# Performance work log

Hardware: AMD Instinct MI355X
Metric: run time of the kernel (lower is better)

## Reference

```python
import jax, jax.numpy as jnp
import numpy as np

EMBED_DIM = 512
NUM_HEADS = 8
HEAD_DIM = EMBED_DIM // NUM_HEADS
SHIFT_INIT = 5.0
EPS = 1e-6


def setup_inputs() -> dict:
    key = jax.random.key(0)
    ks = jax.random.split(key, 8)
    L, N, E = 2048, 4, EMBED_DIM
    query = jax.random.normal(ks[0], (L, N, E), dtype=jnp.float32)
    k_in = jax.random.normal(ks[1], (L, N, E), dtype=jnp.float32)
    v_in = jax.random.normal(ks[2], (L, N, E), dtype=jnp.float32)
    # MultiheadAttention packed projections
    in_proj_weight = jax.random.normal(ks[3], (3 * E, E), dtype=jnp.float32) / np.sqrt(E)
    in_proj_bias = jnp.zeros((3 * E,), dtype=jnp.float32)
    out_proj_weight = jax.random.normal(ks[4], (E, E), dtype=jnp.float32) / np.sqrt(E)
    out_proj_bias = jnp.zeros((E,), dtype=jnp.float32)
    # GeM parameters: p ~ N(1, 0.02), shift = 5
    p = 1.0 + 0.02 * jax.random.normal(ks[5], (E,), dtype=jnp.float32)
    shift = jnp.full((E,), SHIFT_INIT, dtype=jnp.float32)
    return {
        "query": query, "key": k_in, "value": v_in,
        "in_proj_weight": in_proj_weight, "in_proj_bias": in_proj_bias,
        "out_proj_weight": out_proj_weight, "out_proj_bias": out_proj_bias,
        "p": p, "shift": shift,
    }


def reference(query, key, value, in_proj_weight, in_proj_bias,
              out_proj_weight, out_proj_bias, p, shift):
    L, N, E = query.shape
    H, D = NUM_HEADS, HEAD_DIM
    w_q, w_k, w_v = jnp.split(in_proj_weight, 3, axis=0)   # each (E, E)
    b_q, b_k, b_v = jnp.split(in_proj_bias, 3, axis=0)

    def proj(x, w, b):
        # (L, N, E) -> (N, H, L, D)
        y = x @ w.T + b
        return y.reshape(L, N, H, D).transpose(1, 2, 0, 3)

    q = proj(query, w_q, b_q)
    k = proj(key, w_k, b_k)
    v = proj(value, w_v, b_v)

    scale = 1.0 / np.sqrt(D)
    scores = jnp.einsum('nhld,nhsd->nhls', q, k) * scale   # (N,H,L,S)
    attn = jax.nn.softmax(scores, axis=-1)

    # GeM pooling of values: shift -> power p -> weighted mean -> inverse power -> unshift
    p_h = p.reshape(H, D)[None, :, None, :]                # (1,H,1,D)
    shift_h = shift.reshape(H, D)[None, :, None, :]
    v_pos = jnp.maximum(v + shift_h, EPS)                  # keep base positive
    pooled = jnp.einsum('nhls,nhsd->nhld', attn, v_pos ** p_h)
    out_h = jnp.maximum(pooled, EPS) ** (1.0 / p_h) - shift_h  # (N,H,L,D)

    out = out_h.transpose(2, 0, 1, 3).reshape(L, N, E)     # back to (L,N,E)
    out = out @ out_proj_weight.T + out_proj_bias
    return out
```

## Files before the change

### kernel.cpp

```cpp
#include <hip/hip_runtime.h>
#include <hip/hip_bf16.h>

#define E_DIM 512
#define N_BATCH 4
#define L_SEQ 2048
#define N_HEADS 8
#define H_DIM 64
#define N_ROWS (L_SEQ * N_BATCH)
#define EPS_F 1e-6f

typedef __attribute__((ext_vector_type(8))) short bf16x8;
typedef __attribute__((ext_vector_type(4))) float f32x4;
typedef __attribute__((ext_vector_type(16))) float f32x16;

__device__ __forceinline__ void split2(float f, __hip_bfloat16& h, __hip_bfloat16& l) {
  h = __float2bfloat16(f);
  l = __float2bfloat16(f - __bfloat162float(h));
}

__global__ __launch_bounds__(256) void wconv_kernel(
    const float* __restrict__ wio, const float* __restrict__ wo,
    __hip_bfloat16* __restrict__ wiohi, __hip_bfloat16* __restrict__ wiolo,
    __hip_bfloat16* __restrict__ wohi, __hip_bfloat16* __restrict__ wolo) {
  const int g = blockIdx.x * 256 + threadIdx.x;
  const float* src;
  __hip_bfloat16 *dh, *dl;
  int i;
  if (g < 196608) { src = wio; dh = wiohi; dl = wiolo; i = g * 4; }
  else            { src = wo;  dh = wohi;  dl = wolo;  i = (g - 196608) * 4; }
  const float4 f = *(const float4*)(src + i);
  alignas(8) __hip_bfloat16 h[4], l[4];
  split2(f.x, h[0], l[0]); split2(f.y, h[1], l[1]);
  split2(f.z, h[2], l[2]); split2(f.w, h[3], l[3]);
  *(uint2*)(dh + i) = *(const uint2*)h;
  *(uint2*)(dl + i) = *(const uint2*)l;
}

__global__ __launch_bounds__(256, 3) void proj_qkv_kernel(
    const float* __restrict__ xq, const float* __restrict__ xk,
    const float* __restrict__ xv,
    const __hip_bfloat16* __restrict__ whi, const __hip_bfloat16* __restrict__ wlo,
    const float* __restrict__ bias, const float* __restrict__ pw,
    const float* __restrict__ sw,
    __hip_bfloat16* __restrict__ qbuf, __hip_bfloat16* __restrict__ kbuf,
    float* __restrict__ ubuf) {
  __shared__ __hip_bfloat16 Xh[128][40];
  __shared__ __hip_bfloat16 Xl[128][40];
  __shared__ __hip_bfloat16 Wh[128][40];
  __shared__ __hip_bfloat16 Wl[128][40];
  const int z = blockIdx.z;
  const int row0 = blockIdx.x * 128;
  const int col0 = blockIdx.y * 128;
  const float* __restrict__ xsrc = (z == 0) ? xq : (z == 1) ? xk : xv;
  const int tid = threadIdx.x;
  const int lane = tid & 63;
  const int wv = tid >> 6;
  const int lidx = lane & 15;
  const int quad = lane >> 4;
  const int srow = tid >> 1;
  const int scol = (tid & 1) * 16;

  f32x4 acc[2][8];
#pragma unroll
  for (int rt = 0; rt < 2; ++rt)
#pragma unroll
    for (int ct = 0; ct < 8; ++ct) acc[rt][ct] = (f32x4){0.f, 0.f, 0.f, 0.f};

  const int ar0 = wv * 32 + lidx;

  for (int kt = 0; kt < 16; ++kt) {
    const int k0 = kt * 32;
    {
      const float* xp = xsrc + (size_t)(row0 + srow) * E_DIM + k0 + scol;
      float f[16];
      *(float4*)&f[0]  = ((const float4*)xp)[0];
      *(float4*)&f[4]  = ((const float4*)xp)[1];
      *(float4*)&f[8]  = ((const float4*)xp)[2];
      *(float4*)&f[12] = ((const float4*)xp)[3];
      alignas(16) __hip_bfloat16 hi[16], lo[16];
#pragma unroll
      for (int j = 0; j < 16; ++j) split2(f[j], hi[j], lo[j]);
      *(uint4*)&Xh[srow][scol]     = ((const uint4*)hi)[0];
      *(uint4*)&Xh[srow][scol + 8] = ((const uint4*)hi)[1];
      *(uint4*)&Xl[srow][scol]     = ((const uint4*)lo)[0];
      *(uint4*)&Xl[srow][scol + 8] = ((const uint4*)lo)[1];
    }
    {
      const size_t wof = (size_t)(z * E_DIM + col0 + srow) * E_DIM + k0 + scol;
      *(uint4*)&Wh[srow][scol]     = ((const uint4*)(whi + wof))[0];
      *(uint4*)&Wh[srow][scol + 8] = ((const uint4*)(whi + wof))[1];
      *(uint4*)&Wl[srow][scol]     = ((const uint4*)(wlo + wof))[0];
      *(uint4*)&Wl[srow][scol + 8] = ((const uint4*)(wlo + wof))[1];
    }
    __syncthreads();

    const bf16x8 ah0 = *(const bf16x8*)&Xh[ar0][quad * 8];
    const bf16x8 ah1 = *(const bf16x8*)&Xh[ar0 + 16][quad * 8];
    const bf16x8 al0 = *(const bf16x8*)&Xl[ar0][quad * 8];
    const bf16x8 al1 = *(const bf16x8*)&Xl[ar0 + 16][quad * 8];
#pragma unroll
    for (int ct = 0; ct < 8; ++ct) {
      const bf16x8 bh = *(const bf16x8*)&Wh[ct * 16 + lidx][quad * 8];
      const bf16x8 bl = *(const bf16x8*)&Wl[ct * 16 + lidx][quad * 8];
      acc[0][ct] = __builtin_amdgcn_mfma_f32_16x16x32_bf16(ah0, bh, acc[0][ct], 0, 0, 0);
      acc[0][ct] = __builtin_amdgcn_mfma_f32_16x16x32_bf16(al0, bh, acc[0][ct], 0, 0, 0);
      acc[0][ct] = __builtin_amdgcn_mfma_f32_16x16x32_bf16(ah0, bl, acc[0][ct], 0, 0, 0);
      acc[1][ct] = __builtin_amdgcn_mfma_f32_16x16x32_bf16(ah1, bh, acc[1][ct], 0, 0, 0);
      acc[1][ct] = __builtin_amdgcn_mfma_f32_16x16x32_bf16(al1, bh, acc[1][ct], 0, 0, 0);
      acc[1][ct] = __builtin_amdgcn_mfma_f32_16x16x32_bf16(ah1, bl, acc[1][ct], 0, 0, 0);
    }
    __syncthreads();
  }

  if (z < 2) {
    __hip_bfloat16* __restrict__ dst = (z == 0) ? qbuf : kbuf;
    float bv[8];
#pragma unroll
    for (int ct = 0; ct < 8; ++ct) bv[ct] = bias[z * E_DIM + col0 + ct * 16 + lidx];
#pragma unroll
    for (int rt = 0; rt < 2; ++rt)
#pragma unroll
      for (int ct = 0; ct < 8; ++ct) {
        const int e = col0 + ct * 16 + lidx;
        const int h = e >> 6, d = e & 63;
#pragma unroll
        for (int reg = 0; reg < 4; ++reg) {
          const int R = row0 + wv * 32 + rt * 16 + quad * 4 + reg;
          const int lpos = R >> 2, nb = R & 3;
          dst[(((size_t)nb * N_HEADS + h) * L_SEQ + lpos) * H_DIM + d] =
              __float2bfloat16(acc[rt][ct][reg] + bv[ct]);
        }
      }
  } else {
    float bv[8], pv[8], sv[8];
#pragma unroll
    for (int ct = 0; ct < 8; ++ct) {
      const int e = col0 + ct * 16 + lidx;
      bv[ct] = bias[2 * E_DIM + e]; pv[ct] = pw[e]; sv[ct] = sw[e];
    }
#pragma unroll
    for (int rt = 0; rt < 2; ++rt)
#pragma unroll
      for (int ct = 0; ct < 8; ++ct) {
        const int e = col0 + ct * 16 + lidx;
        const int h = e >> 6, d = e & 63;
#pragma unroll
        for (int reg = 0; reg < 4; ++reg) {
          const int R = row0 + wv * 32 + rt * 16 + quad * 4 + reg;
          const int lpos = R >> 2, nb = R & 3;
          const float y = acc[rt][ct][reg] + bv[ct];
          const float vp = fmaxf(y + sv[ct], EPS_F);
          ubuf[(((size_t)nb * N_HEADS + h) * L_SEQ + lpos) * H_DIM + d] =
              __powf(vp, pv[ct]);
        }
      }
  }
}

__global__ __launch_bounds__(256) void transp_kernel(
    const float* __restrict__ u, __hip_bfloat16* __restrict__ uThi,
    __hip_bfloat16* __restrict__ uTlo) {
  __shared__ float T[64][65];
  const int lt = blockIdx.x, h = blockIdx.y, nb = blockIdx.z;
  const int tid = threadIdx.x;
  const int r = tid >> 2;
  const int cb = (tid & 3) * 16;
  const size_t srcbase = ((size_t)nb * N_HEADS + h) * L_SEQ + lt * 64;
  {
    const float* p = u + (srcbase + r) * H_DIM + cb;
    *(float4*)&T[r][cb + 0]  = ((const float4*)p)[0];
    *(float4*)&T[r][cb + 4]  = ((const float4*)p)[1];
    *(float4*)&T[r][cb + 8]  = ((const float4*)p)[2];
    *(float4*)&T[r][cb + 12] = ((const float4*)p)[3];
  }
  __syncthreads();
  alignas(16) __hip_bfloat16 hi[16], lo[16];
#pragma unroll
  for (int j = 0; j < 16; ++j) split2(T[cb + j][r], hi[j], lo[j]);
  const size_t dst = (((size_t)nb * N_HEADS + h) * H_DIM + r) * L_SEQ + lt * 64 + cb;
  *(uint4*)(uThi + dst)     = ((const uint4*)hi)[0];
  *(uint4*)(uThi + dst + 8) = ((const uint4*)hi)[1];
  *(uint4*)(uTlo + dst)     = ((const uint4*)lo)[0];
  *(uint4*)(uTlo + dst + 8) = ((const uint4*)lo)[1];
}

__global__ __launch_bounds__(128, 2) void attn_kernel(
    const __hip_bfloat16* __restrict__ qbuf, const __hip_bfloat16* __restrict__ kbuf,
    const __hip_bfloat16* __restrict__ uThi, const __hip_bfloat16* __restrict__ uTlo,
    const float* __restrict__ pw, const float* __restrict__ sw,
    __hip_bfloat16* __restrict__ ohhi, __hip_bfloat16* __restrict__ ohlo) {
  __shared__ __hip_bfloat16 Ps[64][72];
  __shared__ __hip_bfloat16 Ks[64][72];
  __shared__ __hip_bfloat16 Uh[64][72];
  __shared__ __hip_bfloat16 Ul[64][72];

  const int qt = blockIdx.x, h = blockIdx.y, nb = blockIdx.z;
  const int q0 = qt * 64;
  const int tid = threadIdx.x;
  const int lane = tid & 63;
  const int wv = tid >> 6;
  const int lm = lane & 31;
  const int kg = lane >> 5;
  const int srow = tid >> 1;
  const int scb = (tid & 1) * 32;

  const size_t headbase = ((size_t)nb * N_HEADS + h) * L_SEQ;
  const size_t dbase = ((size_t)nb * N_HEADS + h) * H_DIM;

  {
    const __hip_bfloat16* p = qbuf + (headbase + q0 + srow) * H_DIM + scb;
    *(uint4*)&Ps[srow][scb + 0]  = ((const uint4*)p)[0];
    *(uint4*)&Ps[srow][scb + 8]  = ((const uint4*)p)[1];
    *(uint4*)&Ps[srow][scb + 16] = ((const uint4*)p)[2];
    *(uint4*)&Ps[srow][scb + 24] = ((const uint4*)p)[3];
  }
  __syncthreads();
  bf16x8 aq[4];
#pragma unroll
  for (int kc = 0; kc < 4; ++kc)
    aq[kc] = *(const bf16x8*)&Ps[wv * 32 + lm][kc * 16 + kg * 8];

  bf16x8 ones;
#pragma unroll
  for (int j = 0; j < 8; ++j) ones[j] = (short)0x3F80;

  float pwv[2], swv[2];
#pragma unroll
  for (int nt = 0; nt < 2; ++nt) {
    const int e = h * H_DIM + nt * 32 + lm;
    pwv[nt] = 1.0f / pw[e];
    swv[nt] = sw[e];
  }

  f32x16 o[2], lacc;
  o[0] = (f32x16)(0.f); o[1] = (f32x16)(0.f); lacc = (f32x16)(0.f);

  for (int scn = 0; scn < 32; ++scn) {
    const int s0 = scn * 64;
    __syncthreads();
    {
      const __hip_bfloat16* kp = kbuf + (headbase + s0 + srow) * H_DIM + scb;
      *(uint4*)&Ks[srow][scb + 0]  = ((const uint4*)kp)[0];
      *(uint4*)&Ks[srow][scb + 8]  = ((const uint4*)kp)[1];
      *(uint4*)&Ks[srow][scb + 16] = ((const uint4*)kp)[2];
      *(uint4*)&Ks[srow][scb + 24] = ((const uint4*)kp)[3];
      const __hip_bfloat16* hp = uThi + (dbase + srow) * L_SEQ + s0 + scb;
      *(uint4*)&Uh[srow][scb + 0]  = ((const uint4*)hp)[0];
      *(uint4*)&Uh[srow][scb + 8]  = ((const uint4*)hp)[1];
      *(uint4*)&Uh[srow][scb + 16] = ((const uint4*)hp)[2];
      *(uint4*)&Uh[srow][scb + 24] = ((const uint4*)hp)[3];
      const __hip_bfloat16* lp = uTlo + (dbase + srow) * L_SEQ + s0 + scb;
      *(uint4*)&Ul[srow][scb + 0]  = ((const uint4*)lp)[0];
      *(uint4*)&Ul[srow][scb + 8]  = ((const uint4*)lp)[1];
      *(uint4*)&Ul[srow][scb + 16] = ((const uint4*)lp)[2];
      *(uint4*)&Ul[srow][scb + 24] = ((const uint4*)lp)[3];
    }
    __syncthreads();

    f32x16 sc[2];
#pragma unroll
    for (int nt = 0; nt < 2; ++nt) {
      f32x16 c = (f32x16)(0.f);
#pragma unroll
      for (int kc = 0; kc < 4; ++kc) {
        const bf16x8 bk = *(const bf16x8*)&Ks[nt * 32 + lm][kc * 16 + kg * 8];
        c = __builtin_amdgcn_mfma_f32_32x32x16_bf16(aq[kc], bk, c, 0, 0, 0);
      }
      sc[nt] = c;
    }

#pragma unroll
    for (int nt = 0; nt < 2; ++nt)
#pragma unroll
      for (int reg = 0; reg < 16; ++reg) {
        const float p = __expf(sc[nt][reg] * 0.125f);
        const int row = wv * 32 + (reg & 3) + 8 * (reg >> 2) + 4 * kg;
        Ps[row][nt * 32 + lm] = __float2bfloat16(p);
      }

    bf16x8 ap[4];
#pragma unroll
    for (int kc = 0; kc < 4; ++kc)
      ap[kc] = *(const bf16x8*)&Ps[wv * 32 + lm][kc * 16 + kg * 8];

#pragma unroll
    for (int kc = 0; kc < 4; ++kc)
      lacc = __builtin_amdgcn_mfma_f32_32x32x16_bf16(ap[kc], ones, lacc, 0, 0, 0);

#pragma unroll
    for (int nt = 0; nt < 2; ++nt) {
#pragma unroll
      for (int kc = 0; kc < 4; ++kc) {
        const bf16x8 bh = *(const bf16x8*)&Uh[nt * 32 + lm][kc * 16 + kg * 8];
        o[nt] = __builtin_amdgcn_mfma_f32_32x32x16_bf16(ap[kc], bh, o[nt], 0, 0, 0);
        const bf16x8 bl = *(const bf16x8*)&Ul[nt * 32 + lm][kc * 16 + kg * 8];
        o[nt] = __builtin_amdgcn_mfma_f32_32x32x16_bf16(ap[kc], bl, o[nt], 0, 0, 0);
      }
    }
  }

#pragma unroll
  for (int reg = 0; reg < 16; ++reg) {
    const int row = (reg & 3) + 8 * (reg >> 2) + 4 * kg;
    const int lrow = q0 + wv * 32 + row;
    const float inv = 1.0f / lacc[reg];
#pragma unroll
    for (int nt = 0; nt < 2; ++nt) {
      const int e = h * H_DIM + nt * 32 + lm;
      const float pooled = o[nt][reg] * inv;
      const float val = __powf(fmaxf(pooled, EPS_F), pwv[nt]) - swv[nt];
      __hip_bfloat16 hb, lb;
      split2(val, hb, lb);
      const size_t idx = ((size_t)lrow * N_BATCH + nb) * E_DIM + e;
      ohhi[idx] = hb;
      ohlo[idx] = lb;
    }
  }
}

__global__ __launch_bounds__(256, 4) void out_proj_kernel(
    const __hip_bfloat16* __restrict__ xhi, const __hip_bfloat16* __restrict__ xlo,
    const __hip_bfloat16* __restrict__ whi, const __hip_bfloat16* __restrict__ wlo,
    const float* __restrict__ bias, float* __restrict__ out) {
  __shared__ __hip_bfloat16 Xh[128][40];
  __shared__ __hip_bfloat16 Xl[128][40];
  __shared__ __hip_bfloat16 Wh[64][40];
  __shared__ __hip_bfloat16 Wl[64][40];
  const int row0 = blockIdx.x * 128;
  const int col0 = blockIdx.y * 64;
  const int tid = threadIdx.x;
  const int lane = tid & 63;
  const int wv = tid >> 6;
  const int lidx = lane & 15;
  const int quad = lane >> 4;
  const int srow = tid >> 1;
  const int scol = (tid & 1) * 16;
  const int wrow = tid >> 2;
  const int wcol = (tid & 3) * 8;

  f32x4 acc[2][4];
#pragma unroll
  for (int rt = 0; rt < 2; ++rt)
#pragma unroll
    for (int ct = 0; ct < 4; ++ct) acc[rt][ct] = (f32x4){0.f, 0.f, 0.f, 0.f};

  const int ar0 = wv * 32 + lidx;

  for (int kt = 0; kt < 16; ++kt) {
    const int k0 = kt * 32;
    {
      const size_t xof = (size_t)(row0 + srow) * E_DIM + k0 + scol;
      *(uint4*)&Xh[srow][scol]     = ((const uint4*)(xhi + xof))[0];
      *(uint4*)&Xh[srow][scol + 8] = ((const uint4*)(xhi + xof))[1];
      *(uint4*)&Xl[srow][scol]     = ((const uint4*)(xlo + xof))[0];
      *(uint4*)&Xl[srow][scol + 8] = ((const uint4*)(xlo + xof))[1];
      const size_t wof = (size_t)(col0 + wrow) * E_DIM + k0 + wcol;
      *(uint4*)&Wh[wrow][wcol] = *(const uint4*)(whi + wof);
      *(uint4*)&Wl[wrow][wcol] = *(const uint4*)(wlo + wof);
    }
    __syncthreads();

    const bf16x8 ah0 = *(const bf16x8*)&Xh[ar0][quad * 8];
    const bf16x8 ah1 = *(const bf16x8*)&Xh[ar0 + 16][quad * 8];
    const bf16x8 al0 = *(const bf16x8*)&Xl[ar0][quad * 8];
    const bf16x8 al1 = *(const bf16x8*)&Xl[ar0 + 16][quad * 8];
#pragma unroll
    for (int ct = 0; ct < 4; ++ct) {
      const bf16x8 bh = *(const bf16x8*)&Wh[ct * 16 + lidx][quad * 8];
      const bf16x8 bl = *(const bf16x8*)&Wl[ct * 16 + lidx][quad * 8];
      acc[0][ct] = __builtin_amdgcn_mfma_f32_16x16x32_bf16(ah0, bh, acc[0][ct], 0, 0, 0);
      acc[0][ct] = __builtin_amdgcn_mfma_f32_16x16x32_bf16(al0, bh, acc[0][ct], 0, 0, 0);
      acc[0][ct] = __builtin_amdgcn_mfma_f32_16x16x32_bf16(ah0, bl, acc[0][ct], 0, 0, 0);
      acc[1][ct] = __builtin_amdgcn_mfma_f32_16x16x32_bf16(ah1, bh, acc[1][ct], 0, 0, 0);
      acc[1][ct] = __builtin_amdgcn_mfma_f32_16x16x32_bf16(al1, bh, acc[1][ct], 0, 0, 0);
      acc[1][ct] = __builtin_amdgcn_mfma_f32_16x16x32_bf16(ah1, bl, acc[1][ct], 0, 0, 0);
    }
    __syncthreads();
  }

  float bv[4];
#pragma unroll
  for (int ct = 0; ct < 4; ++ct) bv[ct] = bias[col0 + ct * 16 + lidx];
#pragma unroll
  for (int rt = 0; rt < 2; ++rt)
#pragma unroll
    for (int ct = 0; ct < 4; ++ct) {
      const int c = col0 + ct * 16 + lidx;
#pragma unroll
      for (int reg = 0; reg < 4; ++reg) {
        const int R = row0 + wv * 32 + rt * 16 + quad * 4 + reg;
        out[(size_t)R * E_DIM + c] = acc[rt][ct][reg] + bv[ct];
      }
    }
}

extern "C" void kernel_launch(void* const* d_in, const int* in_sizes, int n_in,
                              void* d_out, int out_size, void* d_ws, size_t ws_size,
                              hipStream_t stream) {
  const float* q_in = (const float*)d_in[0];
  const float* k_in = (const float*)d_in[1];
  const float* v_in = (const float*)d_in[2];
  const float* wio  = (const float*)d_in[3];
  const float* bio  = (const float*)d_in[4];
  const float* wo   = (const float*)d_in[5];
  const float* bo   = (const float*)d_in[6];
  const float* pw   = (const float*)d_in[7];
  const float* sw   = (const float*)d_in[8];

  const size_t NE = (size_t)N_ROWS * E_DIM;
  __hip_bfloat16* qbuf = (__hip_bfloat16*)d_ws;
  __hip_bfloat16* kbuf = qbuf + NE;
  float* ubuf = (float*)(kbuf + NE);
  __hip_bfloat16* uThi = (__hip_bfloat16*)(ubuf + NE);
  __hip_bfloat16* uTlo = uThi + NE;
  __hip_bfloat16* wiohi = uTlo + NE;
  __hip_bfloat16* wiolo = wiohi + 786432;
  __hip_bfloat16* wohi  = wiolo + 786432;
  __hip_bfloat16* wolo  = wohi + 262144;
  __hip_bfloat16* ohhi = (__hip_bfloat16*)ubuf;
  __hip_bfloat16* ohlo = ohhi + NE;

  wconv_kernel<<<dim3(1024), 256, 0, stream>>>(wio, wo, wiohi, wiolo, wohi, wolo);
  proj_qkv_kernel<<<dim3(64, 4, 3), 256, 0, stream>>>(q_in, k_in, v_in, wiohi, wiolo,
                                                      bio, pw, sw, qbuf, kbuf, ubuf);
  transp_kernel<<<dim3(32, 8, 4), 256, 0, stream>>>(ubuf, uThi, uTlo);
  attn_kernel<<<dim3(32, 8, 4), 128, 0, stream>>>(qbuf, kbuf, uThi, uTlo,
                                                  pw, sw, ohhi, ohlo);
  out_proj_kernel<<<dim3(64, 8), 256, 0, stream>>>(ohhi, ohlo, wohi, wolo,
                                                   bo, (float*)d_out);
}
```

Baseline: 301.4 us.

## Switch attention to fp16 MFMA with register-resident probabilities and larger query tiles

```diff
diff --git a/kernel.cpp b/kernel.cpp
--- a/kernel.cpp
+++ b/kernel.cpp
@@ -8,14 +8,23 @@
 #define H_DIM 64
 #define N_ROWS (L_SEQ * N_BATCH)
 #define EPS_F 1e-6f
+#define SC_Q 0.18033688f
 
 typedef __attribute__((ext_vector_type(8))) short bf16x8;
+typedef __attribute__((ext_vector_type(8))) _Float16 f16x8;
 typedef __attribute__((ext_vector_type(4))) float f32x4;
 typedef __attribute__((ext_vector_type(16))) float f32x16;
 
 __device__ __forceinline__ void split2(float f, __hip_bfloat16& h, __hip_bfloat16& l) {
   h = __float2bfloat16(f);
   l = __float2bfloat16(f - __bfloat162float(h));
+}
+
+__device__ __forceinline__ unsigned int packf16(float a, float b) {
+  union { _Float16 h[2]; unsigned int u; } c;
+  c.h[0] = (_Float16)a;
+  c.h[1] = (_Float16)b;
+  return c.u;
 }
 
 __global__ __launch_bounds__(256) void wconv_kernel(
@@ -38,16 +47,14 @@
 
 __global__ __launch_bounds__(256, 3) void proj_qkv_kernel(
     const float* __restrict__ xq, const float* __restrict__ xk,
-    const float* __restrict__ xv,
-    const __hip_bfloat16* __restrict__ whi, const __hip_bfloat16* __restrict__ wlo,
+    const float* __restrict__ xv, const __hip_bfloat16* __restrict__ whi,
     const float* __restrict__ bias, const float* __restrict__ pw,
     const float* __restrict__ sw,
-    __hip_bfloat16* __restrict__ qbuf, __hip_bfloat16* __restrict__ kbuf,
+    _Float16* __restrict__ qbuf, _Float16* __restrict__ kbuf,
     float* __restrict__ ubuf) {
   __shared__ __hip_bfloat16 Xh[128][40];
   __shared__ __hip_bfloat16 Xl[128][40];
   __shared__ __hip_bfloat16 Wh[128][40];
-  __shared__ __hip_bfloat16 Wl[128][40];
   const int z = blockIdx.z;
   const int row0 = blockIdx.x * 128;
   const int col0 = blockIdx.y * 128;
@@ -89,8 +96,6 @@
       const size_t wof = (size_t)(z * E_DIM + col0 + srow) * E_DIM + k0 + scol;
       *(uint4*)&Wh[srow][scol]     = ((const uint4*)(whi + wof))[0];
       *(uint4*)&Wh[srow][scol + 8] = ((const uint4*)(whi + wof))[1];
-      *(uint4*)&Wl[srow][scol]     = ((const uint4*)(wlo + wof))[0];
-      *(uint4*)&Wl[srow][scol + 8] = ((const uint4*)(wlo + wof))[1];
     }
     __syncthreads();
 
@@ -101,19 +106,17 @@
 #pragma unroll
     for (int ct = 0; ct < 8; ++ct) {
       const bf16x8 bh = *(const bf16x8*)&Wh[ct * 16 + lidx][quad * 8];
-      const bf16x8 bl = *(const bf16x8*)&Wl[ct * 16 + lidx][quad * 8];
       acc[0][ct] = __builtin_amdgcn_mfma_f32_16x16x32_bf16(ah0, bh, acc[0][ct], 0, 0, 0);
       acc[0][ct] = __builtin_amdgcn_mfma_f32_16x16x32_bf16(al0, bh, acc[0][ct], 0, 0, 0);
-      acc[0][ct] = __builtin_amdgcn_mfma_f32_16x16x32_bf16(ah0, bl, acc[0][ct], 0, 0, 0);
       acc[1][ct] = __builtin_amdgcn_mfma_f32_16x16x32_bf16(ah1, bh, acc[1][ct], 0, 0, 0);
       acc[1][ct] = __builtin_amdgcn_mfma_f32_16x16x32_bf16(al1, bh, acc[1][ct], 0, 0, 0);
-      acc[1][ct] = __builtin_amdgcn_mfma_f32_16x16x32_bf16(ah1, bl, acc[1][ct], 0, 0, 0);
     }
     __syncthreads();
   }
 
   if (z < 2) {
-    __hip_bfloat16* __restrict__ dst = (z == 0) ? qbuf : kbuf;
+    _Float16* __restrict__ dst = (z == 0) ? qbuf : kbuf;
+    const float scale = (z == 0) ? SC_Q : 1.0f;
     float bv[8];
 #pragma unroll
     for (int ct = 0; ct < 8; ++ct) bv[ct] = bias[z * E_DIM + col0 + ct * 16 + lidx];
@@ -128,7 +131,7 @@
           const int R = row0 + wv * 32 + rt * 16 + quad * 4 + reg;
           const int lpos = R >> 2, nb = R & 3;
           dst[(((size_t)nb * N_HEADS + h) * L_SEQ + lpos) * H_DIM + d] =
-              __float2bfloat16(acc[rt][ct][reg] + bv[ct]);
+              (_Float16)((acc[rt][ct][reg] + bv[ct]) * scale);
         }
       }
   } else {
@@ -158,8 +161,7 @@
 }
 
 __global__ __launch_bounds__(256) void transp_kernel(
-    const float* __restrict__ u, __hip_bfloat16* __restrict__ uThi,
-    __hip_bfloat16* __restrict__ uTlo) {
+    const float* __restrict__ u, _Float16* __restrict__ uT) {
   __shared__ float T[64][65];
   const int lt = blockIdx.x, h = blockIdx.y, nb = blockIdx.z;
   const int tid = threadIdx.x;
@@ -174,28 +176,23 @@
     *(float4*)&T[r][cb + 12] = ((const float4*)p)[3];
   }
   __syncthreads();
-  alignas(16) __hip_bfloat16 hi[16], lo[16];
-#pragma unroll
-  for (int j = 0; j < 16; ++j) split2(T[cb + j][r], hi[j], lo[j]);
+  alignas(16) _Float16 hv[16];
+#pragma unroll
+  for (int j = 0; j < 16; ++j) hv[j] = (_Float16)T[cb + j][r];
   const size_t dst = (((size_t)nb * N_HEADS + h) * H_DIM + r) * L_SEQ + lt * 64 + cb;
-  *(uint4*)(uThi + dst)     = ((const uint4*)hi)[0];
-  *(uint4*)(uThi + dst + 8) = ((const uint4*)hi)[1];
-  *(uint4*)(uTlo + dst)     = ((const uint4*)lo)[0];
-  *(uint4*)(uTlo + dst + 8) = ((const uint4*)lo)[1];
+  *(uint4*)(uT + dst)     = ((const uint4*)hv)[0];
+  *(uint4*)(uT + dst + 8) = ((const uint4*)hv)[1];
 }
 
 __global__ __launch_bounds__(128, 2) void attn_kernel(
-    const __hip_bfloat16* __restrict__ qbuf, const __hip_bfloat16* __restrict__ kbuf,
-    const __hip_bfloat16* __restrict__ uThi, const __hip_bfloat16* __restrict__ uTlo,
-    const float* __restrict__ pw, const float* __restrict__ sw,
-    __hip_bfloat16* __restrict__ ohhi, __hip_bfloat16* __restrict__ ohlo) {
-  __shared__ __hip_bfloat16 Ps[64][72];
-  __shared__ __hip_bfloat16 Ks[64][72];
-  __shared__ __hip_bfloat16 Uh[64][72];
-  __shared__ __hip_bfloat16 Ul[64][72];
-
+    const _Float16* __restrict__ qbuf, const _Float16* __restrict__ kbuf,
+    const _Float16* __restrict__ uT, const float* __restrict__ pw,
+    const float* __restrict__ sw, __hip_bfloat16* __restrict__ ohhi,
+    __hip_bfloat16* __restrict__ ohlo) {
+  __shared__ _Float16 Ks[64][72];
+  __shared__ _Float16 Us[64][72];
   const int qt = blockIdx.x, h = blockIdx.y, nb = blockIdx.z;
-  const int q0 = qt * 64;
+  const int q0 = qt * 128;
   const int tid = threadIdx.x;
   const int lane = tid & 63;
   const int wv = tid >> 6;
@@ -203,118 +200,115 @@
   const int kg = lane >> 5;
   const int srow = tid >> 1;
   const int scb = (tid & 1) * 32;
-
   const size_t headbase = ((size_t)nb * N_HEADS + h) * L_SEQ;
   const size_t dbase = ((size_t)nb * N_HEADS + h) * H_DIM;
 
-  {
-    const __hip_bfloat16* p = qbuf + (headbase + q0 + srow) * H_DIM + scb;
-    *(uint4*)&Ps[srow][scb + 0]  = ((const uint4*)p)[0];
-    *(uint4*)&Ps[srow][scb + 8]  = ((const uint4*)p)[1];
-    *(uint4*)&Ps[srow][scb + 16] = ((const uint4*)p)[2];
-    *(uint4*)&Ps[srow][scb + 24] = ((const uint4*)p)[3];
-  }
-  __syncthreads();
-  bf16x8 aq[4];
-#pragma unroll
-  for (int kc = 0; kc < 4; ++kc)
-    aq[kc] = *(const bf16x8*)&Ps[wv * 32 + lm][kc * 16 + kg * 8];
-
-  bf16x8 ones;
-#pragma unroll
-  for (int j = 0; j < 8; ++j) ones[j] = (short)0x3F80;
-
-  float pwv[2], swv[2];
-#pragma unroll
-  for (int nt = 0; nt < 2; ++nt) {
-    const int e = h * H_DIM + nt * 32 + lm;
-    pwv[nt] = 1.0f / pw[e];
-    swv[nt] = sw[e];
-  }
-
-  f32x16 o[2], lacc;
-  o[0] = (f32x16)(0.f); o[1] = (f32x16)(0.f); lacc = (f32x16)(0.f);
+  f16x8 bq[2][4];
+#pragma unroll
+  for (int nt = 0; nt < 2; ++nt)
+#pragma unroll
+    for (int kc = 0; kc < 4; ++kc)
+      bq[nt][kc] = *(const f16x8*)(qbuf +
+          (headbase + q0 + wv * 64 + nt * 32 + lm) * H_DIM + kc * 16 + kg * 8);
+
+  f32x16 o[2][2];
+  o[0][0] = (f32x16)(0.f); o[0][1] = (f32x16)(0.f);
+  o[1][0] = (f32x16)(0.f); o[1][1] = (f32x16)(0.f);
+  float lsum[2] = {0.f, 0.f};
 
   for (int scn = 0; scn < 32; ++scn) {
     const int s0 = scn * 64;
     __syncthreads();
     {
-      const __hip_bfloat16* kp = kbuf + (headbase + s0 + srow) * H_DIM + scb;
+      const _Float16* kp = kbuf + (headbase + s0 + srow) * H_DIM + scb;
       *(uint4*)&Ks[srow][scb + 0]  = ((const uint4*)kp)[0];
       *(uint4*)&Ks[srow][scb + 8]  = ((const uint4*)kp)[1];
       *(uint4*)&Ks[srow][scb + 16] = ((const uint4*)kp)[2];
       *(uint4*)&Ks[srow][scb + 24] = ((const uint4*)kp)[3];
-      const __hip_bfloat16* hp = uThi + (dbase + srow) * L_SEQ + s0 + scb;
-      *(uint4*)&Uh[srow][scb + 0]  = ((const uint4*)hp)[0];
-      *(uint4*)&Uh[srow][scb + 8]  = ((const uint4*)hp)[1];
-      *(uint4*)&Uh[srow][scb + 16] = ((const uint4*)hp)[2];
-      *(uint4*)&Uh[srow][scb + 24] = ((const uint4*)hp)[3];
-      const __hip_bfloat16* lp = uTlo + (dbase + srow) * L_SEQ + s0 + scb;
-      *(uint4*)&Ul[srow][scb + 0]  = ((const uint4*)lp)[0];
-      *(uint4*)&Ul[srow][scb + 8]  = ((const uint4*)lp)[1];
-      *(uint4*)&Ul[srow][scb + 16] = ((const uint4*)lp)[2];
-      *(uint4*)&Ul[srow][scb + 24] = ((const uint4*)lp)[3];
-    }
-    __syncthreads();
-
-    f32x16 sc[2];
-#pragma unroll
-    for (int nt = 0; nt < 2; ++nt) {
-      f32x16 c = (f32x16)(0.f);
-#pragma unroll
-      for (int kc = 0; kc < 4; ++kc) {
-        const bf16x8 bk = *(const bf16x8*)&Ks[nt * 32 + lm][kc * 16 + kg * 8];
-        c = __builtin_amdgcn_mfma_f32_32x32x16_bf16(aq[kc], bk, c, 0, 0, 0);
+      const _Float16* up = uT + (dbase + srow) * L_SEQ + s0 + scb;
+      *(uint4*)&Us[srow][scb + 0]  = ((const uint4*)up)[0];
+      *(uint4*)&Us[srow][scb + 8]  = ((const uint4*)up)[1];
+      *(uint4*)&Us[srow][scb + 16] = ((const uint4*)up)[2];
+      *(uint4*)&Us[srow][scb + 24] = ((const uint4*)up)[3];
+    }
+    __syncthreads();
+
+    f32x16 sc[2][2];
+    sc[0][0] = (f32x16)(0.f); sc[0][1] = (f32x16)(0.f);
+    sc[1][0] = (f32x16)(0.f); sc[1][1] = (f32x16)(0.f);
+#pragma unroll
+    for (int kc = 0; kc < 4; ++kc) {
+      const f16x8 ak0 = *(const f16x8*)&Ks[lm][kc * 16 + kg * 8];
+      const f16x8 ak1 = *(const f16x8*)&Ks[32 + lm][kc * 16 + kg * 8];
+      sc[0][0] = __builtin_amdgcn_mfma_f32_32x32x16_f16(ak0, bq[0][kc], sc[0][0], 0, 0, 0);
+      sc[0][1] = __builtin_amdgcn_mfma_f32_32x32x16_f16(ak1, bq[0][kc], sc[0][1], 0, 0, 0);
+      sc[1][0] = __builtin_amdgcn_mfma_f32_32x32x16_f16(ak0, bq[1][kc], sc[1][0], 0, 0, 0);
+      sc[1][1] = __builtin_amdgcn_mfma_f32_32x32x16_f16(ak1, bq[1][kc], sc[1][1], 0, 0, 0);
+    }
+
+    unsigned int P2[2][2][4][2];
+#pragma unroll
+    for (int nt = 0; nt < 2; ++nt)
+#pragma unroll
+      for (int mt = 0; mt < 2; ++mt)
+#pragma unroll
+        for (int g = 0; g < 4; ++g) {
+          const float p0 = __builtin_amdgcn_exp2f(sc[nt][mt][4 * g + 0]);
+          const float p1 = __builtin_amdgcn_exp2f(sc[nt][mt][4 * g + 1]);
+          const float p2 = __builtin_amdgcn_exp2f(sc[nt][mt][4 * g + 2]);
+          const float p3 = __builtin_amdgcn_exp2f(sc[nt][mt][4 * g + 3]);
+          lsum[nt] += (p0 + p1) + (p2 + p3);
+          P2[nt][mt][g][0] = packf16(p0, p1);
+          P2[nt][mt][g][1] = packf16(p2, p3);
+        }
+
+#pragma unroll
+    for (int kc = 0; kc < 4; ++kc) {
+      const int mt = kc >> 1;
+      const f16x8 au0 = *(const f16x8*)&Us[lm][kc * 16 + kg * 8];
+      const f16x8 au1 = *(const f16x8*)&Us[32 + lm][kc * 16 + kg * 8];
+#pragma unroll
+      for (int nt = 0; nt < 2; ++nt) {
+        const int gx = (2 * kc) & 3, gy = (2 * kc + 1) & 3;
+        const unsigned int x0 = P2[nt][mt][gx][0], x1 = P2[nt][mt][gx][1];
+        const unsigned int y0 = P2[nt][mt][gy][0], y1 = P2[nt][mt][gy][1];
+        const unsigned int sA = kg ? x0 : y0, sB = kg ? x1 : y1;
+        const unsigned int rA = (unsigned int)__shfl_xor((int)sA, 32);
+        const unsigned int rB = (unsigned int)__shfl_xor((int)sB, 32);
+        union { unsigned int u[4]; f16x8 v; } bp;
+        bp.u[0] = kg ? rA : x0;
+        bp.u[1] = kg ? rB : x1;
+        bp.u[2] = kg ? y0 : rA;
+        bp.u[3] = kg ? y1 : rB;
+        o[nt][0] = __builtin_amdgcn_mfma_f32_32x32x16_f16(au0, bp.v, o[nt][0], 0, 0, 0);
+        o[nt][1] = __builtin_amdgcn_mfma_f32_32x32x16_f16(au1, bp.v, o[nt][1], 0, 0, 0);
       }
-      sc[nt] = c;
-    }
-
-#pragma unroll
-    for (int nt = 0; nt < 2; ++nt)
-#pragma unroll
-      for (int reg = 0; reg < 16; ++reg) {
-        const float p = __expf(sc[nt][reg] * 0.125f);
-        const int row = wv * 32 + (reg & 3) + 8 * (reg >> 2) + 4 * kg;
-        Ps[row][nt * 32 + lm] = __float2bfloat16(p);
+    }
+  }
+
+#pragma unroll
+  for (int nt = 0; nt < 2; ++nt) {
+    const float l = lsum[nt] + __shfl_xor(lsum[nt], 32);
+    const float inv = 1.0f / l;
+    const int qg = q0 + wv * 64 + nt * 32 + lm;
+    const size_t base = ((size_t)qg * N_BATCH + nb) * E_DIM + h * H_DIM;
+#pragma unroll
+    for (int mt2 = 0; mt2 < 2; ++mt2)
+#pragma unroll
+      for (int g = 0; g < 4; ++g) {
+        alignas(8) __hip_bfloat16 hb[4], lb[4];
+#pragma unroll
+        for (int i = 0; i < 4; ++i) {
+          const int d = mt2 * 32 + 8 * g + 4 * kg + i;
+          const int e = h * H_DIM + d;
+          const float pooled = o[nt][mt2][4 * g + i] * inv;
+          const float val = __powf(fmaxf(pooled, EPS_F), 1.0f / pw[e]) - sw[e];
+          split2(val, hb[i], lb[i]);
+        }
+        const int d0 = mt2 * 32 + 8 * g + 4 * kg;
+        *(uint2*)(ohhi + base + d0) = *(const uint2*)hb;
+        *(uint2*)(ohlo + base + d0) = *(const uint2*)lb;
       }
-
-    bf16x8 ap[4];
-#pragma unroll
-    for (int kc = 0; kc < 4; ++kc)
-      ap[kc] = *(const bf16x8*)&Ps[wv * 32 + lm][kc * 16 + kg * 8];
-
-#pragma unroll
-    for (int kc = 0; kc < 4; ++kc)
-      lacc = __builtin_amdgcn_mfma_f32_32x32x16_bf16(ap[kc], ones, lacc, 0, 0, 0);
-
-#pragma unroll
-    for (int nt = 0; nt < 2; ++nt) {
-#pragma unroll
-      for (int kc = 0; kc < 4; ++kc) {
-        const bf16x8 bh = *(const bf16x8*)&Uh[nt * 32 + lm][kc * 16 + kg * 8];
-        o[nt] = __builtin_amdgcn_mfma_f32_32x32x16_bf16(ap[kc], bh, o[nt], 0, 0, 0);
-        const bf16x8 bl = *(const bf16x8*)&Ul[nt * 32 + lm][kc * 16 + kg * 8];
-        o[nt] = __builtin_amdgcn_mfma_f32_32x32x16_bf16(ap[kc], bl, o[nt], 0, 0, 0);
-      }
-    }
-  }
-
-#pragma unroll
-  for (int reg = 0; reg < 16; ++reg) {
-    const int row = (reg & 3) + 8 * (reg >> 2) + 4 * kg;
-    const int lrow = q0 + wv * 32 + row;
-    const float inv = 1.0f / lacc[reg];
-#pragma unroll
-    for (int nt = 0; nt < 2; ++nt) {
-      const int e = h * H_DIM + nt * 32 + lm;
-      const float pooled = o[nt][reg] * inv;
-      const float val = __powf(fmaxf(pooled, EPS_F), pwv[nt]) - swv[nt];
-      __hip_bfloat16 hb, lb;
-      split2(val, hb, lb);
-      const size_t idx = ((size_t)lrow * N_BATCH + nb) * E_DIM + e;
-      ohhi[idx] = hb;
-      ohlo[idx] = lb;
-    }
   }
 }
 
@@ -408,12 +402,11 @@
   const float* sw   = (const float*)d_in[8];
 
   const size_t NE = (size_t)N_ROWS * E_DIM;
-  __hip_bfloat16* qbuf = (__hip_bfloat16*)d_ws;
-  __hip_bfloat16* kbuf = qbuf + NE;
+  _Float16* qbuf = (_Float16*)d_ws;
+  _Float16* kbuf = qbuf + NE;
   float* ubuf = (float*)(kbuf + NE);
-  __hip_bfloat16* uThi = (__hip_bfloat16*)(ubuf + NE);
-  __hip_bfloat16* uTlo = uThi + NE;
-  __hip_bfloat16* wiohi = uTlo + NE;
+  _Float16* uT = (_Float16*)(ubuf + NE);
+  __hip_bfloat16* wiohi = (__hip_bfloat16*)(uT + NE);
   __hip_bfloat16* wiolo = wiohi + 786432;
   __hip_bfloat16* wohi  = wiolo + 786432;
   __hip_bfloat16* wolo  = wohi + 262144;
@@ -421,11 +414,11 @@
   __hip_bfloat16* ohlo = ohhi + NE;
 
   wconv_kernel<<<dim3(1024), 256, 0, stream>>>(wio, wo, wiohi, wiolo, wohi, wolo);
-  proj_qkv_kernel<<<dim3(64, 4, 3), 256, 0, stream>>>(q_in, k_in, v_in, wiohi, wiolo,
+  proj_qkv_kernel<<<dim3(64, 4, 3), 256, 0, stream>>>(q_in, k_in, v_in, wiohi,
                                                       bio, pw, sw, qbuf, kbuf, ubuf);
-  transp_kernel<<<dim3(32, 8, 4), 256, 0, stream>>>(ubuf, uThi, uTlo);
-  attn_kernel<<<dim3(32, 8, 4), 128, 0, stream>>>(qbuf, kbuf, uThi, uTlo,
-                                                  pw, sw, ohhi, ohlo);
+  transp_kernel<<<dim3(32, 8, 4), 256, 0, stream>>>(ubuf, uT);
+  attn_kernel<<<dim3(16, 8, 4), 128, 0, stream>>>(qbuf, kbuf, uT, pw, sw,
+                                                  ohhi, ohlo);
   out_proj_kernel<<<dim3(64, 8), 256, 0, stream>>>(ohhi, ohlo, wohi, wolo,
                                                    bo, (float*)d_out);
 }
```

Result: faster. 288.7 us (-4.2%).
